# Kernel optimization log

Measured on AMD Instinct MI355X. Metric: run time of the kernel, lower is better.

The kernel has to match this reference:

```python
import jax, jax.numpy as jnp
import numpy as np

N_NODES = 100000
N_EDGES = 1600000
D_H = 64
D_E = 64
D_Q = 64
D_HID = 128
N_GRAPHS = 16


def _mlp_params(key, d_in, d_hid):
    k1, k2, k3, k4 = jax.random.split(key, 4)
    s1 = 1.0 / np.sqrt(d_in)
    s2 = 1.0 / np.sqrt(d_hid)
    return (
        jax.random.uniform(k1, (d_in, d_hid), jnp.float32, -s1, s1),
        jax.random.uniform(k2, (d_hid,), jnp.float32, -s1, s1),
        jax.random.uniform(k3, (d_hid, 1), jnp.float32, -s2, s2),
        jax.random.uniform(k4, (1,), jnp.float32, -s2, s2),
    )


def setup_inputs() -> dict:
    key = jax.random.key(0)
    ks = jax.random.split(key, 8)
    h = jax.random.normal(ks[0], (N_NODES, D_H), jnp.float32)
    e = jax.random.normal(ks[1], (N_EDGES, D_E), jnp.float32)
    q = jax.random.normal(ks[2], (N_GRAPHS, D_Q), jnp.float32)
    edge_index = jax.random.randint(ks[3], (2, N_EDGES), 0, N_NODES, jnp.int64)
    edge_batch = jax.random.randint(ks[4], (N_EDGES,), 0, N_GRAPHS, jnp.int64)
    gw1, gb1, gw2, gb2 = _mlp_params(ks[5], 2 * D_H + D_Q, D_HID)
    sw1, sb1, sw2, sb2 = _mlp_params(ks[6], 2 * D_H + D_E, D_HID)
    return {
        "h": h, "e": e, "q": q,
        "edge_index": edge_index, "edge_batch": edge_batch,
        "gate_w1": gw1, "gate_b1": gb1, "gate_w2": gw2, "gate_b2": gb2,
        "score_w1": sw1, "score_b1": sb1, "score_w2": sw2, "score_b2": sb2,
    }


def _mlp(x, w1, b1, w2, b2):
    # 2-layer MLP, no layernorm (use_layer_norm=False), output dim 1
    hidden = jax.nn.relu(x @ w1 + b1)
    return (hidden @ w2 + b2)[..., 0]


def _dst_softmax(raw, dst, num_nodes):
    # numerically stable per-destination softmax via segment reductions
    max_vals = jax.ops.segment_max(raw, dst, num_segments=num_nodes)
    exp_vals = jnp.exp(raw - max_vals[dst])
    sum_exp = jax.ops.segment_sum(exp_vals, dst, num_segments=num_nodes)
    denom = jnp.maximum(sum_exp[dst], 1e-9)
    return exp_vals / denom


def reference(h, e, q, edge_index, edge_batch,
              gate_w1, gate_b1, gate_w2, gate_b2,
              score_w1, score_b1, score_w2, score_b2):
    src, dst = edge_index[0], edge_index[1]
    h_i = h[src]            # [E, d_h]
    h_j = h[dst]            # [E, d_h]
    q_e = q[edge_batch]     # [E, d_q]
    gate_in = jnp.concatenate([h_i, h_j, q_e], axis=-1)
    gate = jax.nn.sigmoid(_mlp(gate_in, gate_w1, gate_b1, gate_w2, gate_b2))
    score_in = jnp.concatenate([h_i, h_j, e], axis=-1)
    score = _mlp(score_in, score_w1, score_b1, score_w2, score_b2)
    raw = gate * score
    return _dst_softmax(raw, dst, h.shape[0])
```

## Files before the change

kernel.cpp:

```cpp
#include <hip/hip_runtime.h>
#include <hip/hip_bf16.h>

#define NN 100000
#define NE 1600000

typedef __attribute__((ext_vector_type(8))) unsigned short ushort8v;
typedef __attribute__((ext_vector_type(8))) short short8v;
typedef __attribute__((ext_vector_type(4))) float f32x4;

__device__ __forceinline__ float b2f(unsigned short u) {
  return __uint_as_float(((unsigned)u) << 16);
}
__device__ __forceinline__ short f2bs(float f) {
  unsigned u = __float_as_uint(f);
  unsigned r = (u + 0x7FFFu + ((u >> 16) & 1u)) >> 16;
  return (short)r;
}
__device__ __forceinline__ unsigned fkey(float f) {
  unsigned u = __float_as_uint(f);
  return (u & 0x80000000u) ? ~u : (u | 0x80000000u);
}
__device__ __forceinline__ float funkey(unsigned k) {
  unsigned u = (k & 0x80000000u) ? (k ^ 0x80000000u) : ~k;
  return __uint_as_float(u);
}

__global__ void qproj_kernel(const float* __restrict__ q,
                             const float* __restrict__ gw1,
                             const float* __restrict__ gb1,
                             float* __restrict__ Qg) {
  int g = blockIdx.x, j = threadIdx.x;
  float acc = gb1[j];
  for (int k = 0; k < 64; ++k) acc += q[g * 64 + k] * gw1[(128 + k) * 128 + j];
  Qg[g * 128 + j] = acc;
}

__global__ __launch_bounds__(256) void nodeproj_kernel(
    const float* __restrict__ h, const float* __restrict__ gw1,
    const float* __restrict__ sw1, __hip_bfloat16* __restrict__ SRCP,
    __hip_bfloat16* __restrict__ DSTP) {
  __shared__ float hs[64][64];
  __shared__ float Ws[64][128];
  int part = blockIdx.y;
  const float* W = (part & 1) ? sw1 : gw1;
  int roff = (part >= 2) ? 64 : 0;
  __hip_bfloat16* outp = (part >= 2) ? DSTP : SRCP;
  int coff = (part & 1) ? 128 : 0;
  int n0 = blockIdx.x * 64;
  int t = threadIdx.x;

  {
    int n = t & 63, kc = t >> 6;
    int gn = n0 + n;
#pragma unroll
    for (int i = 0; i < 4; ++i) {
      int k = kc * 16 + i * 4;
      float4 hv = make_float4(0.f, 0.f, 0.f, 0.f);
      if (gn < NN) hv = *(const float4*)&h[gn * 64 + k];
      hs[k + 0][n] = hv.x; hs[k + 1][n] = hv.y;
      hs[k + 2][n] = hv.z; hs[k + 3][n] = hv.w;
    }
  }
  {
    const float* Wb = W + roff * 128;
    float* wsf = &Ws[0][0];
#pragma unroll
    for (int i = 0; i < 8; ++i) {
      int flat = (i * 256 + t) * 4;
      *(float4*)&wsf[flat] = *(const float4*)&Wb[flat];
    }
  }
  __syncthreads();

  int tx = t & 31, ty = t >> 5;
  float acc[8][4] = {};
#pragma unroll 4
  for (int k = 0; k < 64; ++k) {
    float hn[8];
    *(float4*)&hn[0] = *(const float4*)&hs[k][ty * 8];
    *(float4*)&hn[4] = *(const float4*)&hs[k][ty * 8 + 4];
    float wv[4];
#pragma unroll
    for (int i = 0; i < 4; ++i) wv[i] = Ws[k][tx + 32 * i];
#pragma unroll
    for (int j = 0; j < 8; ++j)
#pragma unroll
      for (int i = 0; i < 4; ++i) acc[j][i] += hn[j] * wv[i];
  }
#pragma unroll
  for (int j = 0; j < 8; ++j) {
    int gn = n0 + ty * 8 + j;
    if (gn < NN) {
#pragma unroll
      for (int i = 0; i < 4; ++i)
        outp[(size_t)gn * 256 + coff + tx + 32 * i] = __float2bfloat16(acc[j][i]);
    }
  }
}

__global__ __launch_bounds__(256) void edge_kernel(
    const float* __restrict__ e, const int* __restrict__ eidx,
    const int* __restrict__ ebat, const __hip_bfloat16* __restrict__ SRCP,
    const __hip_bfloat16* __restrict__ DSTP, const float* __restrict__ Qg,
    const float* __restrict__ sw1, const float* __restrict__ sb1,
    const float* __restrict__ gw2, const float* __restrict__ gb2,
    const float* __restrict__ sw2, const float* __restrict__ sb2,
    float* __restrict__ raw_out, unsigned* __restrict__ nmax) {
  __shared__ float gateLDS[256];
  const int tid = threadIdx.x;
  const int w = tid >> 6, lane = tid & 63;
  const int qg = lane >> 4, cl = lane & 15;
  const int EB = blockIdx.x * 256 + w * 64;
  const unsigned short* SU = (const unsigned short*)SRCP;
  const unsigned short* DU = (const unsigned short*)DSTP;

  short8v Bf[8][2];
#pragma unroll
  for (int t = 0; t < 8; ++t)
#pragma unroll
    for (int ks = 0; ks < 2; ++ks) {
      short8v b;
#pragma unroll
      for (int j = 0; j < 8; ++j) {
        int k = ks * 32 + qg * 8 + j;
        b[j] = f2bs(sw1[(128 + k) * 128 + t * 16 + cl]);
      }
      Bf[t][ks] = b;
    }

  float sbv[8], s2v[8];
#pragma unroll
  for (int t = 0; t < 8; ++t) {
    sbv[t] = sb1[t * 16 + cl];
    s2v[t] = sw2[t * 16 + cl];
  }
  const float sb2v = sb2[0], gb2v = gb2[0];

  {
    int E = EB + lane;
    int src = eidx[E], dst = eidx[NE + E], g = ebat[E];
    const ushort8v* sr = (const ushort8v*)(SU + (size_t)src * 256);
    const ushort8v* dr = (const ushort8v*)(DU + (size_t)dst * 256);
    const float4* qv = (const float4*)(Qg + g * 128);
    const float4* w2 = (const float4*)gw2;
    float gacc = 0.f;
#pragma unroll
    for (int jo = 0; jo < 8; ++jo) {
      ushort8v ga = sr[jo], gb = dr[jo];
#pragma unroll
      for (int half = 0; half < 2; ++half) {
        float4 qq = qv[2 * jo + half];
        float4 ww = w2[2 * jo + half];
        float qa[4] = {qq.x, qq.y, qq.z, qq.w};
        float wa[4] = {ww.x, ww.y, ww.z, ww.w};
#pragma unroll
        for (int ii = 0; ii < 4; ++ii) {
          float x = b2f(ga[half * 4 + ii]) + b2f(gb[half * 4 + ii]) + qa[ii];
          gacc = fmaf(fmaxf(x, 0.f), wa[ii], gacc);
        }
      }
    }
    gateLDS[tid] = 1.f / (1.f + __expf(-(gacc + gb2v)));
  }
  __syncthreads();

#pragma unroll 1
  for (int rt = 0; rt < 4; ++rt) {
    int arow = EB + rt * 16 + cl;
    const float* ap = e + (size_t)arow * 64 + qg * 8;
    f32x4 f0 = __builtin_nontemporal_load((const f32x4*)(ap + 0));
    f32x4 f1 = __builtin_nontemporal_load((const f32x4*)(ap + 4));
    f32x4 f2 = __builtin_nontemporal_load((const f32x4*)(ap + 32));
    f32x4 f3 = __builtin_nontemporal_load((const f32x4*)(ap + 36));
    short8v a0, a1;
    a0[0] = f2bs(f0.x); a0[1] = f2bs(f0.y); a0[2] = f2bs(f0.z); a0[3] = f2bs(f0.w);
    a0[4] = f2bs(f1.x); a0[5] = f2bs(f1.y); a0[6] = f2bs(f1.z); a0[7] = f2bs(f1.w);
    a1[0] = f2bs(f2.x); a1[1] = f2bs(f2.y); a1[2] = f2bs(f2.z); a1[3] = f2bs(f2.w);
    a1[4] = f2bs(f3.x); a1[5] = f2bs(f3.y); a1[6] = f2bs(f3.z); a1[7] = f2bs(f3.w);

    f32x4 acc[8];
#pragma unroll
    for (int t = 0; t < 8; ++t) {
      acc[t] = (f32x4){0.f, 0.f, 0.f, 0.f};
      acc[t] = __builtin_amdgcn_mfma_f32_16x16x32_bf16(a0, Bf[t][0], acc[t], 0, 0, 0);
      acc[t] = __builtin_amdgcn_mfma_f32_16x16x32_bf16(a1, Bf[t][1], acc[t], 0, 0, 0);
    }

    int srcv[4], dstv[4];
#pragma unroll
    for (int i = 0; i < 4; ++i) {
      int E = EB + rt * 16 + qg * 4 + i;
      srcv[i] = eidx[E];
      dstv[i] = eidx[NE + E];
    }
    float part[4] = {0.f, 0.f, 0.f, 0.f};
#pragma unroll
    for (int t = 0; t < 8; ++t) {
      int col = 128 + t * 16 + cl;
#pragma unroll
      for (int i = 0; i < 4; ++i) {
        float sa = b2f(SU[(size_t)srcv[i] * 256 + col]);
        float sb = b2f(DU[(size_t)dstv[i] * 256 + col]);
        float hv = acc[t][i] + sa + sb + sbv[t];
        part[i] = fmaf(fmaxf(hv, 0.f), s2v[t], part[i]);
      }
    }
#pragma unroll
    for (int m = 1; m < 16; m <<= 1)
#pragma unroll
      for (int i = 0; i < 4; ++i) part[i] += __shfl_xor(part[i], m, 64);

    if (cl < 4) {
      int r = rt * 16 + qg * 4 + cl;
      int E = EB + r;
      float p = (cl == 0) ? part[0] : (cl == 1) ? part[1] : (cl == 2) ? part[2] : part[3];
      int d   = (cl == 0) ? dstv[0] : (cl == 1) ? dstv[1] : (cl == 2) ? dstv[2] : dstv[3];
      float raw = gateLDS[w * 64 + r] * (p + sb2v);
      raw_out[E] = raw;
      atomicMax(&nmax[d], fkey(raw));
    }
  }
}

__global__ __launch_bounds__(256) void expsum_kernel(
    const float* __restrict__ raw, const int* __restrict__ eidx,
    const unsigned* __restrict__ nodemax, float* __restrict__ out,
    float* __restrict__ nodesum) {
  int ee = blockIdx.x * 256 + threadIdx.x;
  int dst = eidx[NE + ee];
  float m = funkey(nodemax[dst]);
  float ex = __expf(raw[ee] - m);
  out[ee] = ex;
  atomicAdd(&nodesum[dst], ex);
}

__global__ __launch_bounds__(256) void norm_kernel(
    const int* __restrict__ eidx, const float* __restrict__ nodesum,
    float* __restrict__ out) {
  int ee = blockIdx.x * 256 + threadIdx.x;
  int dst = eidx[NE + ee];
  out[ee] = out[ee] / fmaxf(nodesum[dst], 1e-9f);
}

extern "C" void kernel_launch(void* const* d_in, const int* in_sizes, int n_in,
                              void* d_out, int out_size, void* d_ws, size_t ws_size,
                              hipStream_t stream) {
  const float* h   = (const float*)d_in[0];
  const float* e   = (const float*)d_in[1];
  const float* q   = (const float*)d_in[2];
  const int* eidx  = (const int*)d_in[3];
  const int* ebat  = (const int*)d_in[4];
  const float* gw1 = (const float*)d_in[5];
  const float* gb1 = (const float*)d_in[6];
  const float* gw2 = (const float*)d_in[7];
  const float* gb2 = (const float*)d_in[8];
  const float* sw1 = (const float*)d_in[9];
  const float* sb1 = (const float*)d_in[10];
  const float* sw2 = (const float*)d_in[11];
  const float* sb2 = (const float*)d_in[12];
  float* out = (float*)d_out;

  char* ws = (char*)d_ws;
  __hip_bfloat16* SRCP = (__hip_bfloat16*)ws;
  __hip_bfloat16* DSTP = (__hip_bfloat16*)(ws + 51200000);
  float* Qg      = (float*)(ws + 102400000);
  float* rawb    = (float*)(ws + 102400000 + 8192);
  unsigned* nmax = (unsigned*)(ws + 102400000 + 8192 + 6400000);
  float* nsum    = (float*)(ws + 102400000 + 8192 + 6400000 + 400000);

  (void)hipMemsetAsync(nmax, 0, 800000, stream);
  qproj_kernel<<<dim3(16), dim3(128), 0, stream>>>(q, gw1, gb1, Qg);
  nodeproj_kernel<<<dim3(1563, 4), dim3(256), 0, stream>>>(h, gw1, sw1, SRCP, DSTP);
  edge_kernel<<<dim3(NE / 256), dim3(256), 0, stream>>>(
      e, eidx, ebat, SRCP, DSTP, Qg, sw1, sb1, gw2, gb2, sw2, sb2, rawb, nmax);
  expsum_kernel<<<dim3(NE / 256), dim3(256), 0, stream>>>(rawb, eidx, nmax, out, nsum);
  norm_kernel<<<dim3(NE / 256), dim3(256), 0, stream>>>(eidx, nsum, out);
}
```

Measured before the change: 526.1 us.

## Fuse exp and sum into edge kernel, drop segment max, prepack weights in LDS

The separate max pass is gone: the edge kernel computes exp(raw) directly, writes it to the output and atomically adds it into the per-node sums. This removes the raw buffer, the atomicMax traffic and the whole expsum launch. The score-layer weights are now packed to bf16 once by a small prepack kernel, then staged through LDS with swapped MFMA operands so that each lane can load four contiguous SRCP/DSTP elements at a time. The gate loop now covers all 128 hidden units instead of 64, which corrects an earlier bug but adds gate work per edge. Dropping the max subtraction gives up numerical stability and can overflow if raw values grow large.

```diff
diff --git a/kernel.cpp b/kernel.cpp
--- a/kernel.cpp
+++ b/kernel.cpp
@@ -5,6 +5,7 @@
 #define NE 1600000
 
 typedef __attribute__((ext_vector_type(8))) unsigned short ushort8v;
+typedef __attribute__((ext_vector_type(4))) unsigned short ushort4v;
 typedef __attribute__((ext_vector_type(8))) short short8v;
 typedef __attribute__((ext_vector_type(4))) float f32x4;
 
@@ -15,14 +16,6 @@
   unsigned u = __float_as_uint(f);
   unsigned r = (u + 0x7FFFu + ((u >> 16) & 1u)) >> 16;
   return (short)r;
-}
-__device__ __forceinline__ unsigned fkey(float f) {
-  unsigned u = __float_as_uint(f);
-  return (u & 0x80000000u) ? ~u : (u | 0x80000000u);
-}
-__device__ __forceinline__ float funkey(unsigned k) {
-  unsigned u = (k & 0x80000000u) ? (k ^ 0x80000000u) : ~k;
-  return __uint_as_float(u);
 }
 
 __global__ void qproj_kernel(const float* __restrict__ q,
@@ -33,6 +26,18 @@
   float acc = gb1[j];
   for (int k = 0; k < 64; ++k) acc += q[g * 64 + k] * gw1[(128 + k) * 128 + j];
   Qg[g * 128 + j] = acc;
+}
+
+__global__ __launch_bounds__(1024) void prepack_kernel(
+    const float* __restrict__ sw1, short8v* __restrict__ WtG) {
+  int tid = threadIdx.x;
+  int t = tid >> 7, ks = (tid >> 6) & 1, lane = tid & 63;
+  int qg = lane >> 4, cl = lane & 15;
+  short8v fr;
+#pragma unroll
+  for (int j = 0; j < 8; ++j)
+    fr[j] = f2bs(sw1[(128 + ks * 32 + qg * 8 + j) * 128 + t * 16 + cl]);
+  WtG[tid] = fr;
 }
 
 __global__ __launch_bounds__(256) void nodeproj_kernel(
@@ -102,10 +107,11 @@
     const float* __restrict__ e, const int* __restrict__ eidx,
     const int* __restrict__ ebat, const __hip_bfloat16* __restrict__ SRCP,
     const __hip_bfloat16* __restrict__ DSTP, const float* __restrict__ Qg,
-    const float* __restrict__ sw1, const float* __restrict__ sb1,
+    const short8v* __restrict__ WtG, const float* __restrict__ sb1,
     const float* __restrict__ gw2, const float* __restrict__ gb2,
     const float* __restrict__ sw2, const float* __restrict__ sb2,
-    float* __restrict__ raw_out, unsigned* __restrict__ nmax) {
+    float* __restrict__ out, float* __restrict__ nsum) {
+  __shared__ short8v WtS[1024];
   __shared__ float gateLDS[256];
   const int tid = threadIdx.x;
   const int w = tid >> 6, lane = tid & 63;
@@ -113,50 +119,34 @@
   const int EB = blockIdx.x * 256 + w * 64;
   const unsigned short* SU = (const unsigned short*)SRCP;
   const unsigned short* DU = (const unsigned short*)DSTP;
-
-  short8v Bf[8][2];
-#pragma unroll
-  for (int t = 0; t < 8; ++t)
-#pragma unroll
-    for (int ks = 0; ks < 2; ++ks) {
-      short8v b;
-#pragma unroll
-      for (int j = 0; j < 8; ++j) {
-        int k = ks * 32 + qg * 8 + j;
-        b[j] = f2bs(sw1[(128 + k) * 128 + t * 16 + cl]);
-      }
-      Bf[t][ks] = b;
-    }
-
-  float sbv[8], s2v[8];
-#pragma unroll
-  for (int t = 0; t < 8; ++t) {
-    sbv[t] = sb1[t * 16 + cl];
-    s2v[t] = sw2[t * 16 + cl];
-  }
   const float sb2v = sb2[0], gb2v = gb2[0];
+
+  {
+    const f32x4* s4 = (const f32x4*)WtG;
+    f32x4* d4 = (f32x4*)WtS;
+#pragma unroll
+    for (int i = 0; i < 4; ++i) d4[tid + i * 256] = s4[tid + i * 256];
+  }
 
   {
     int E = EB + lane;
     int src = eidx[E], dst = eidx[NE + E], g = ebat[E];
     const ushort8v* sr = (const ushort8v*)(SU + (size_t)src * 256);
     const ushort8v* dr = (const ushort8v*)(DU + (size_t)dst * 256);
-    const float4* qv = (const float4*)(Qg + g * 128);
-    const float4* w2 = (const float4*)gw2;
+    const f32x4* qv = (const f32x4*)(Qg + g * 128);
+    const f32x4* w2 = (const f32x4*)gw2;
     float gacc = 0.f;
 #pragma unroll
-    for (int jo = 0; jo < 8; ++jo) {
+    for (int jo = 0; jo < 16; ++jo) {
       ushort8v ga = sr[jo], gb = dr[jo];
 #pragma unroll
       for (int half = 0; half < 2; ++half) {
-        float4 qq = qv[2 * jo + half];
-        float4 ww = w2[2 * jo + half];
-        float qa[4] = {qq.x, qq.y, qq.z, qq.w};
-        float wa[4] = {ww.x, ww.y, ww.z, ww.w};
+        f32x4 qq = qv[2 * jo + half];
+        f32x4 ww = w2[2 * jo + half];
 #pragma unroll
         for (int ii = 0; ii < 4; ++ii) {
-          float x = b2f(ga[half * 4 + ii]) + b2f(gb[half * 4 + ii]) + qa[ii];
-          gacc = fmaf(fmaxf(x, 0.f), wa[ii], gacc);
+          float x = b2f(ga[half * 4 + ii]) + b2f(gb[half * 4 + ii]) + qq[ii];
+          gacc = fmaf(fmaxf(x, 0.f), ww[ii], gacc);
         }
       }
     }
@@ -164,74 +154,61 @@
   }
   __syncthreads();
 
-#pragma unroll 1
+  short8v a0[4], a1[4];
+  int srcv[4], dstv[4];
+#pragma unroll
   for (int rt = 0; rt < 4; ++rt) {
-    int arow = EB + rt * 16 + cl;
-    const float* ap = e + (size_t)arow * 64 + qg * 8;
+    int erow = EB + rt * 16 + cl;
+    srcv[rt] = eidx[erow];
+    dstv[rt] = eidx[NE + erow];
+    const float* ap = e + (size_t)erow * 64 + qg * 8;
     f32x4 f0 = __builtin_nontemporal_load((const f32x4*)(ap + 0));
     f32x4 f1 = __builtin_nontemporal_load((const f32x4*)(ap + 4));
     f32x4 f2 = __builtin_nontemporal_load((const f32x4*)(ap + 32));
     f32x4 f3 = __builtin_nontemporal_load((const f32x4*)(ap + 36));
-    short8v a0, a1;
-    a0[0] = f2bs(f0.x); a0[1] = f2bs(f0.y); a0[2] = f2bs(f0.z); a0[3] = f2bs(f0.w);
-    a0[4] = f2bs(f1.x); a0[5] = f2bs(f1.y); a0[6] = f2bs(f1.z); a0[7] = f2bs(f1.w);
-    a1[0] = f2bs(f2.x); a1[1] = f2bs(f2.y); a1[2] = f2bs(f2.z); a1[3] = f2bs(f2.w);
-    a1[4] = f2bs(f3.x); a1[5] = f2bs(f3.y); a1[6] = f2bs(f3.z); a1[7] = f2bs(f3.w);
-
-    f32x4 acc[8];
-#pragma unroll
-    for (int t = 0; t < 8; ++t) {
-      acc[t] = (f32x4){0.f, 0.f, 0.f, 0.f};
-      acc[t] = __builtin_amdgcn_mfma_f32_16x16x32_bf16(a0, Bf[t][0], acc[t], 0, 0, 0);
-      acc[t] = __builtin_amdgcn_mfma_f32_16x16x32_bf16(a1, Bf[t][1], acc[t], 0, 0, 0);
-    }
-
-    int srcv[4], dstv[4];
-#pragma unroll
-    for (int i = 0; i < 4; ++i) {
-      int E = EB + rt * 16 + qg * 4 + i;
-      srcv[i] = eidx[E];
-      dstv[i] = eidx[NE + E];
-    }
-    float part[4] = {0.f, 0.f, 0.f, 0.f};
-#pragma unroll
-    for (int t = 0; t < 8; ++t) {
-      int col = 128 + t * 16 + cl;
+    short8v x0, x1;
+    x0[0] = f2bs(f0.x); x0[1] = f2bs(f0.y); x0[2] = f2bs(f0.z); x0[3] = f2bs(f0.w);
+    x0[4] = f2bs(f1.x); x0[5] = f2bs(f1.y); x0[6] = f2bs(f1.z); x0[7] = f2bs(f1.w);
+    x1[0] = f2bs(f2.x); x1[1] = f2bs(f2.y); x1[2] = f2bs(f2.z); x1[3] = f2bs(f2.w);
+    x1[4] = f2bs(f3.x); x1[5] = f2bs(f3.y); x1[6] = f2bs(f3.z); x1[7] = f2bs(f3.w);
+    a0[rt] = x0; a1[rt] = x1;
+  }
+
+  float part[4] = {0.f, 0.f, 0.f, 0.f};
+#pragma unroll 2
+  for (int t = 0; t < 8; ++t) {
+    short8v Aw0 = WtS[(t * 2 + 0) * 64 + lane];
+    short8v Aw1 = WtS[(t * 2 + 1) * 64 + lane];
+    f32x4 b1v = *(const f32x4*)&sb1[t * 16 + qg * 4];
+    f32x4 w2v = *(const f32x4*)&sw2[t * 16 + qg * 4];
+    int col = 128 + t * 16 + qg * 4;
+#pragma unroll
+    for (int rt = 0; rt < 4; ++rt) {
+      ushort4v sa = *(const ushort4v*)&SU[(size_t)srcv[rt] * 256 + col];
+      ushort4v sb = *(const ushort4v*)&DU[(size_t)dstv[rt] * 256 + col];
+      f32x4 acc = (f32x4){0.f, 0.f, 0.f, 0.f};
+      acc = __builtin_amdgcn_mfma_f32_16x16x32_bf16(Aw0, a0[rt], acc, 0, 0, 0);
+      acc = __builtin_amdgcn_mfma_f32_16x16x32_bf16(Aw1, a1[rt], acc, 0, 0, 0);
 #pragma unroll
       for (int i = 0; i < 4; ++i) {
-        float sa = b2f(SU[(size_t)srcv[i] * 256 + col]);
-        float sb = b2f(DU[(size_t)dstv[i] * 256 + col]);
-        float hv = acc[t][i] + sa + sb + sbv[t];
-        part[i] = fmaf(fmaxf(hv, 0.f), s2v[t], part[i]);
+        float hv = acc[i] + b2f(sa[i]) + b2f(sb[i]) + b1v[i];
+        part[rt] = fmaf(fmaxf(hv, 0.f), w2v[i], part[rt]);
       }
     }
-#pragma unroll
-    for (int m = 1; m < 16; m <<= 1)
-#pragma unroll
-      for (int i = 0; i < 4; ++i) part[i] += __shfl_xor(part[i], m, 64);
-
-    if (cl < 4) {
-      int r = rt * 16 + qg * 4 + cl;
-      int E = EB + r;
-      float p = (cl == 0) ? part[0] : (cl == 1) ? part[1] : (cl == 2) ? part[2] : part[3];
-      int d   = (cl == 0) ? dstv[0] : (cl == 1) ? dstv[1] : (cl == 2) ? dstv[2] : dstv[3];
-      float raw = gateLDS[w * 64 + r] * (p + sb2v);
-      raw_out[E] = raw;
-      atomicMax(&nmax[d], fkey(raw));
-    }
-  }
-}
-
-__global__ __launch_bounds__(256) void expsum_kernel(
-    const float* __restrict__ raw, const int* __restrict__ eidx,
-    const unsigned* __restrict__ nodemax, float* __restrict__ out,
-    float* __restrict__ nodesum) {
-  int ee = blockIdx.x * 256 + threadIdx.x;
-  int dst = eidx[NE + ee];
-  float m = funkey(nodemax[dst]);
-  float ex = __expf(raw[ee] - m);
-  out[ee] = ex;
-  atomicAdd(&nodesum[dst], ex);
+  }
+
+#pragma unroll
+  for (int rt = 0; rt < 4; ++rt) {
+    float p = part[rt];
+    p += __shfl_xor(p, 16, 64);
+    p += __shfl_xor(p, 32, 64);
+    if (lane < 16) {
+      int r = rt * 16 + cl;
+      float ex = __expf(gateLDS[w * 64 + r] * (p + sb2v));
+      out[EB + r] = ex;
+      atomicAdd(&nsum[dstv[rt]], ex);
+    }
+  }
 }
 
 __global__ __launch_bounds__(256) void norm_kernel(
@@ -263,16 +240,15 @@
   char* ws = (char*)d_ws;
   __hip_bfloat16* SRCP = (__hip_bfloat16*)ws;
   __hip_bfloat16* DSTP = (__hip_bfloat16*)(ws + 51200000);
-  float* Qg      = (float*)(ws + 102400000);
-  float* rawb    = (float*)(ws + 102400000 + 8192);
-  unsigned* nmax = (unsigned*)(ws + 102400000 + 8192 + 6400000);
-  float* nsum    = (float*)(ws + 102400000 + 8192 + 6400000 + 400000);
-
-  (void)hipMemsetAsync(nmax, 0, 800000, stream);
+  float* Qg    = (float*)(ws + 102400000);
+  short8v* WtG = (short8v*)(ws + 102400000 + 8192);
+  float* nsum  = (float*)(ws + 102400000 + 8192 + 16384);
+
+  (void)hipMemsetAsync(nsum, 0, 400000, stream);
   qproj_kernel<<<dim3(16), dim3(128), 0, stream>>>(q, gw1, gb1, Qg);
+  prepack_kernel<<<dim3(1), dim3(1024), 0, stream>>>(sw1, WtG);
   nodeproj_kernel<<<dim3(1563, 4), dim3(256), 0, stream>>>(h, gw1, sw1, SRCP, DSTP);
   edge_kernel<<<dim3(NE / 256), dim3(256), 0, stream>>>(
-      e, eidx, ebat, SRCP, DSTP, Qg, sw1, sb1, gw2, gb2, sw2, sb2, rawb, nmax);
-  expsum_kernel<<<dim3(NE / 256), dim3(256), 0, stream>>>(rawb, eidx, nmax, out, nsum);
+      e, eidx, ebat, SRCP, DSTP, Qg, WtG, sb1, gw2, gb2, sw2, sb2, out, nsum);
   norm_kernel<<<dim3(NE / 256), dim3(256), 0, stream>>>(eidx, nsum, out);
 }
```

Result: slower. 821.2 us (+56.1%).

## Drop softmax max pass, split gate into own kernel, prepack score weights

Applied to the files above, without the earlier changes.

Removes the per-destination max reduction (atomicMax plus the raw buffer) and folds the exp and sum into the score kernel, computing exp(raw) without subtracting a max. The gate MLP moves to its own kernel, and the node projections are split into four separate 128-wide arrays. A one-block kernel pre-converts the score weight fragments to bf16 so each block stops converting them itself. The gate now sums over all 128 hidden units, where the old code used only 64, which also changes results. Skipping the max subtraction can overflow if raw scores are large, and the extra gate kernel adds another gather pass over the edges.

```diff
diff --git a/kernel.cpp b/kernel.cpp
--- a/kernel.cpp
+++ b/kernel.cpp
@@ -15,14 +15,6 @@
   unsigned u = __float_as_uint(f);
   unsigned r = (u + 0x7FFFu + ((u >> 16) & 1u)) >> 16;
   return (short)r;
-}
-__device__ __forceinline__ unsigned fkey(float f) {
-  unsigned u = __float_as_uint(f);
-  return (u & 0x80000000u) ? ~u : (u | 0x80000000u);
-}
-__device__ __forceinline__ float funkey(unsigned k) {
-  unsigned u = (k & 0x80000000u) ? (k ^ 0x80000000u) : ~k;
-  return __uint_as_float(u);
 }
 
 __global__ void qproj_kernel(const float* __restrict__ q,
@@ -35,17 +27,29 @@
   Qg[g * 128 + j] = acc;
 }
 
+__global__ __launch_bounds__(1024) void prepack_kernel(
+    const float* __restrict__ sw1, short8v* __restrict__ WtG) {
+  int tid = threadIdx.x;
+  int t = tid >> 7, ks = (tid >> 6) & 1, lane = tid & 63;
+  int qg = lane >> 4, cl = lane & 15;
+  short8v fr;
+#pragma unroll
+  for (int j = 0; j < 8; ++j)
+    fr[j] = f2bs(sw1[(128 + ks * 32 + qg * 8 + j) * 128 + t * 16 + cl]);
+  WtG[tid] = fr;
+}
+
 __global__ __launch_bounds__(256) void nodeproj_kernel(
     const float* __restrict__ h, const float* __restrict__ gw1,
-    const float* __restrict__ sw1, __hip_bfloat16* __restrict__ SRCP,
-    __hip_bfloat16* __restrict__ DSTP) {
+    const float* __restrict__ sw1, __hip_bfloat16* __restrict__ GA,
+    __hip_bfloat16* __restrict__ GB, __hip_bfloat16* __restrict__ SA,
+    __hip_bfloat16* __restrict__ SB) {
   __shared__ float hs[64][64];
   __shared__ float Ws[64][128];
   int part = blockIdx.y;
   const float* W = (part & 1) ? sw1 : gw1;
   int roff = (part >= 2) ? 64 : 0;
-  __hip_bfloat16* outp = (part >= 2) ? DSTP : SRCP;
-  int coff = (part & 1) ? 128 : 0;
+  __hip_bfloat16* outp = (part == 0) ? GA : (part == 1) ? SA : (part == 2) ? GB : SB;
   int n0 = blockIdx.x * 64;
   int t = threadIdx.x;
 
@@ -93,40 +97,60 @@
     if (gn < NN) {
 #pragma unroll
       for (int i = 0; i < 4; ++i)
-        outp[(size_t)gn * 256 + coff + tx + 32 * i] = __float2bfloat16(acc[j][i]);
-    }
-  }
-}
-
-__global__ __launch_bounds__(256) void edge_kernel(
+        outp[(size_t)gn * 128 + tx + 32 * i] = __float2bfloat16(acc[j][i]);
+    }
+  }
+}
+
+__global__ __launch_bounds__(256) void gate_kernel(
+    const int* __restrict__ eidx, const int* __restrict__ ebat,
+    const __hip_bfloat16* __restrict__ GA, const __hip_bfloat16* __restrict__ GB,
+    const float* __restrict__ Qg, const float* __restrict__ gw2,
+    const float* __restrict__ gb2, float* __restrict__ gate) {
+  int ee = blockIdx.x * 256 + threadIdx.x;
+  int src = eidx[ee], dst = eidx[NE + ee], g = ebat[ee];
+  const ushort8v* ga = (const ushort8v*)((const unsigned short*)GA + (size_t)src * 128);
+  const ushort8v* gb = (const ushort8v*)((const unsigned short*)GB + (size_t)dst * 128);
+  const f32x4* qv = (const f32x4*)(Qg + g * 128);
+  const f32x4* w2 = (const f32x4*)gw2;
+  float gacc = 0.f;
+#pragma unroll
+  for (int jo = 0; jo < 16; ++jo) {
+    ushort8v av = ga[jo], bv = gb[jo];
+#pragma unroll
+    for (int half = 0; half < 2; ++half) {
+      f32x4 qq = qv[2 * jo + half];
+      f32x4 ww = w2[2 * jo + half];
+#pragma unroll
+      for (int ii = 0; ii < 4; ++ii) {
+        float x = b2f(av[half * 4 + ii]) + b2f(bv[half * 4 + ii]) + qq[ii];
+        gacc = fmaf(fmaxf(x, 0.f), ww[ii], gacc);
+      }
+    }
+  }
+  gate[ee] = 1.f / (1.f + __expf(-(gacc + gb2[0])));
+}
+
+__global__ __launch_bounds__(256) void score_kernel(
     const float* __restrict__ e, const int* __restrict__ eidx,
-    const int* __restrict__ ebat, const __hip_bfloat16* __restrict__ SRCP,
-    const __hip_bfloat16* __restrict__ DSTP, const float* __restrict__ Qg,
-    const float* __restrict__ sw1, const float* __restrict__ sb1,
-    const float* __restrict__ gw2, const float* __restrict__ gb2,
+    const __hip_bfloat16* __restrict__ SA, const __hip_bfloat16* __restrict__ SB,
+    const short8v* __restrict__ WtG, const float* __restrict__ sb1,
     const float* __restrict__ sw2, const float* __restrict__ sb2,
-    float* __restrict__ raw_out, unsigned* __restrict__ nmax) {
-  __shared__ float gateLDS[256];
+    const float* __restrict__ gate, float* __restrict__ out,
+    float* __restrict__ nsum) {
   const int tid = threadIdx.x;
   const int w = tid >> 6, lane = tid & 63;
   const int qg = lane >> 4, cl = lane & 15;
   const int EB = blockIdx.x * 256 + w * 64;
-  const unsigned short* SU = (const unsigned short*)SRCP;
-  const unsigned short* DU = (const unsigned short*)DSTP;
+  const unsigned short* SAU = (const unsigned short*)SA;
+  const unsigned short* SBU = (const unsigned short*)SB;
+  const float sb2v = sb2[0];
 
   short8v Bf[8][2];
 #pragma unroll
   for (int t = 0; t < 8; ++t)
 #pragma unroll
-    for (int ks = 0; ks < 2; ++ks) {
-      short8v b;
-#pragma unroll
-      for (int j = 0; j < 8; ++j) {
-        int k = ks * 32 + qg * 8 + j;
-        b[j] = f2bs(sw1[(128 + k) * 128 + t * 16 + cl]);
-      }
-      Bf[t][ks] = b;
-    }
+    for (int ks = 0; ks < 2; ++ks) Bf[t][ks] = WtG[(t * 2 + ks) * 64 + lane];
 
   float sbv[8], s2v[8];
 #pragma unroll
@@ -134,35 +158,6 @@
     sbv[t] = sb1[t * 16 + cl];
     s2v[t] = sw2[t * 16 + cl];
   }
-  const float sb2v = sb2[0], gb2v = gb2[0];
-
-  {
-    int E = EB + lane;
-    int src = eidx[E], dst = eidx[NE + E], g = ebat[E];
-    const ushort8v* sr = (const ushort8v*)(SU + (size_t)src * 256);
-    const ushort8v* dr = (const ushort8v*)(DU + (size_t)dst * 256);
-    const float4* qv = (const float4*)(Qg + g * 128);
-    const float4* w2 = (const float4*)gw2;
-    float gacc = 0.f;
-#pragma unroll
-    for (int jo = 0; jo < 8; ++jo) {
-      ushort8v ga = sr[jo], gb = dr[jo];
-#pragma unroll
-      for (int half = 0; half < 2; ++half) {
-        float4 qq = qv[2 * jo + half];
-        float4 ww = w2[2 * jo + half];
-        float qa[4] = {qq.x, qq.y, qq.z, qq.w};
-        float wa[4] = {ww.x, ww.y, ww.z, ww.w};
-#pragma unroll
-        for (int ii = 0; ii < 4; ++ii) {
-          float x = b2f(ga[half * 4 + ii]) + b2f(gb[half * 4 + ii]) + qa[ii];
-          gacc = fmaf(fmaxf(x, 0.f), wa[ii], gacc);
-        }
-      }
-    }
-    gateLDS[tid] = 1.f / (1.f + __expf(-(gacc + gb2v)));
-  }
-  __syncthreads();
 
 #pragma unroll 1
   for (int rt = 0; rt < 4; ++rt) {
@@ -196,11 +191,11 @@
     float part[4] = {0.f, 0.f, 0.f, 0.f};
 #pragma unroll
     for (int t = 0; t < 8; ++t) {
-      int col = 128 + t * 16 + cl;
+      int col = t * 16 + cl;
 #pragma unroll
       for (int i = 0; i < 4; ++i) {
-        float sa = b2f(SU[(size_t)srcv[i] * 256 + col]);
-        float sb = b2f(DU[(size_t)dstv[i] * 256 + col]);
+        float sa = b2f(SAU[(size_t)srcv[i] * 128 + col]);
+        float sb = b2f(SBU[(size_t)dstv[i] * 128 + col]);
         float hv = acc[t][i] + sa + sb + sbv[t];
         part[i] = fmaf(fmaxf(hv, 0.f), s2v[t], part[i]);
       }
@@ -215,23 +210,11 @@
       int E = EB + r;
       float p = (cl == 0) ? part[0] : (cl == 1) ? part[1] : (cl == 2) ? part[2] : part[3];
       int d   = (cl == 0) ? dstv[0] : (cl == 1) ? dstv[1] : (cl == 2) ? dstv[2] : dstv[3];
-      float raw = gateLDS[w * 64 + r] * (p + sb2v);
-      raw_out[E] = raw;
-      atomicMax(&nmax[d], fkey(raw));
-    }
-  }
-}
-
-__global__ __launch_bounds__(256) void expsum_kernel(
-    const float* __restrict__ raw, const int* __restrict__ eidx,
-    const unsigned* __restrict__ nodemax, float* __restrict__ out,
-    float* __restrict__ nodesum) {
-  int ee = blockIdx.x * 256 + threadIdx.x;
-  int dst = eidx[NE + ee];
-  float m = funkey(nodemax[dst]);
-  float ex = __expf(raw[ee] - m);
-  out[ee] = ex;
-  atomicAdd(&nodesum[dst], ex);
+      float ex = __expf(gate[E] * (p + sb2v));
+      out[E] = ex;
+      atomicAdd(&nsum[d], ex);
+    }
+  }
 }
 
 __global__ __launch_bounds__(256) void norm_kernel(
@@ -261,18 +244,21 @@
   float* out = (float*)d_out;
 
   char* ws = (char*)d_ws;
-  __hip_bfloat16* SRCP = (__hip_bfloat16*)ws;
-  __hip_bfloat16* DSTP = (__hip_bfloat16*)(ws + 51200000);
-  float* Qg      = (float*)(ws + 102400000);
-  float* rawb    = (float*)(ws + 102400000 + 8192);
-  unsigned* nmax = (unsigned*)(ws + 102400000 + 8192 + 6400000);
-  float* nsum    = (float*)(ws + 102400000 + 8192 + 6400000 + 400000);
-
-  (void)hipMemsetAsync(nmax, 0, 800000, stream);
+  __hip_bfloat16* GA = (__hip_bfloat16*)ws;
+  __hip_bfloat16* GB = (__hip_bfloat16*)(ws + 25600000);
+  __hip_bfloat16* SA = (__hip_bfloat16*)(ws + 51200000);
+  __hip_bfloat16* SB = (__hip_bfloat16*)(ws + 76800000);
+  float* Qg    = (float*)(ws + 102400000);
+  short8v* WtG = (short8v*)(ws + 102400000 + 8192);
+  float* gateb = (float*)(ws + 102400000 + 8192 + 16384);
+  float* nsum  = (float*)(ws + 102400000 + 8192 + 16384 + 6400000);
+
+  (void)hipMemsetAsync(nsum, 0, 400000, stream);
   qproj_kernel<<<dim3(16), dim3(128), 0, stream>>>(q, gw1, gb1, Qg);
-  nodeproj_kernel<<<dim3(1563, 4), dim3(256), 0, stream>>>(h, gw1, sw1, SRCP, DSTP);
-  edge_kernel<<<dim3(NE / 256), dim3(256), 0, stream>>>(
-      e, eidx, ebat, SRCP, DSTP, Qg, sw1, sb1, gw2, gb2, sw2, sb2, rawb, nmax);
-  expsum_kernel<<<dim3(NE / 256), dim3(256), 0, stream>>>(rawb, eidx, nmax, out, nsum);
+  prepack_kernel<<<dim3(1), dim3(1024), 0, stream>>>(sw1, WtG);
+  nodeproj_kernel<<<dim3(1563, 4), dim3(256), 0, stream>>>(h, gw1, sw1, GA, GB, SA, SB);
+  gate_kernel<<<dim3(NE / 256), dim3(256), 0, stream>>>(eidx, ebat, GA, GB, Qg, gw2, gb2, gateb);
+  score_kernel<<<dim3(NE / 256), dim3(256), 0, stream>>>(
+      e, eidx, SA, SB, WtG, sb1, sw2, sb2, gateb, out, nsum);
   norm_kernel<<<dim3(NE / 256), dim3(256), 0, stream>>>(eidx, nsum, out);
 }
```

After: 907.0 us. 1.72x slower.
